# Performance work log

Measured on AMD Instinct MI355X. Metric: run time of the kernel, lower is better.

## Reference

```python
import jax, jax.numpy as jnp
import numpy as np

N, E, G = 100000, 400000, 4096
D, H, C, L = 128, 8, 16, 4  # hidden, heads, per-head dim, layers
EPS_BN = 1e-5


def _seg_sum(v, idx, n):
    return jax.ops.segment_sum(v, idx, num_segments=n)


def _seg_max(v, idx, n):
    return jax.ops.segment_max(v, idx, num_segments=n)


def setup_inputs() -> dict:
    key = jax.random.key(0)
    ks = jax.random.split(key, 32)
    rn = lambda k, s, sc=0.1: jax.random.normal(k, s, jnp.float32) * sc
    inp = {
        "x": jax.random.normal(ks[0], (N, 9), jnp.float32),
        "edge_attr": jax.random.normal(ks[1], (E, 3), jnp.float32),
        "edge_index": jax.random.randint(ks[2], (2, E), 0, N, jnp.int32),
        "batch": jnp.sort(jax.random.randint(ks[3], (N,), 0, G, jnp.int32)),
        "W_node": rn(ks[4], (9, D)), "b_node": jnp.zeros((D,), jnp.float32),
        "W_edge": rn(ks[5], (3, D)), "b_edge": jnp.zeros((D,), jnp.float32),
        "W_lin": rn(ks[6], (L, D, D)),
        "att_src": rn(ks[7], (L, H, C)), "att_dst": rn(ks[8], (L, H, C)),
        "W_eproj": rn(ks[9], (L, D, D)), "att_edge": rn(ks[10], (L, H, C)),
        "gat_bias": jnp.zeros((L, D), jnp.float32),
        "bn_gamma": jnp.ones((L, D), jnp.float32), "bn_beta": jnp.zeros((L, D), jnp.float32),
        "gate_W1": rn(ks[11], (D, D // 2)), "gate_b1": jnp.zeros((D // 2,), jnp.float32),
        "gate_W2": rn(ks[12], (D // 2, 1)), "gate_b2": jnp.zeros((1,), jnp.float32),
        "mlp_W1": rn(ks[13], (3 * D, 2 * D)), "mlp_b1": jnp.zeros((2 * D,), jnp.float32),
        "mlp_W2": rn(ks[14], (2 * D, D)), "mlp_b2": jnp.zeros((D,), jnp.float32),
    }
    return inp


def _forward(x, edge_attr, edge_index, batch, W_node, b_node, W_edge, b_edge,
             W_lin, att_src, att_dst, W_eproj, att_edge, gat_bias,
             bn_gamma, bn_beta, gate_W1, gate_b1, gate_W2, gate_b2,
             mlp_W1, mlp_b1, mlp_W2, mlp_b2):
    src, dst = edge_index[0], edge_index[1]
    h = x @ W_node + b_node                         # [N, D]
    e = edge_attr @ W_edge + b_edge                 # [E, D]

    # PyG add_self_loops(fill_value='mean'): self-loop edge feature = mean of
    # incoming edge features at each node.
    deg = _seg_sum(jnp.ones((E,), e.dtype), dst, N)           # [N]
    self_e = _seg_sum(e, dst, N) / jnp.clip(deg, 1.0)[:, None]  # [N, D]
    ar = jnp.arange(N, dtype=src.dtype)
    src_f = jnp.concatenate([src, ar])              # [E+N]
    dst_f = jnp.concatenate([dst, ar])
    e_f = jnp.concatenate([e, self_e], axis=0)      # [E+N, D]

    residual = h
    for l in range(L):
        hp = (h @ W_lin[l]).reshape(N, H, C)                     # [N, H, C]
        a_s = jnp.sum(hp * att_src[l], axis=-1)                  # [N, H]
        a_d = jnp.sum(hp * att_dst[l], axis=-1)                  # [N, H]
        ep = (e_f @ W_eproj[l]).reshape(-1, H, C)                # [E+N, H, C]
        a_e = jnp.sum(ep * att_edge[l], axis=-1)                 # [E+N, H]
        alpha = a_s[src_f] + a_d[dst_f] + a_e
        alpha = jax.nn.leaky_relu(alpha, negative_slope=0.2)
        # segment softmax over edges incident to each destination node
        m = _seg_max(alpha, dst_f, N)
        alpha = jnp.exp(alpha - m[dst_f])
        s = _seg_sum(alpha, dst_f, N)
        alpha = alpha / (s[dst_f] + 1e-16)                       # [E+N, H]
        msg = hp[src_f] * alpha[:, :, None]                      # [E+N, H, C]
        out = _seg_sum(msg, dst_f, N).reshape(N, D) + gat_bias[l]
        # BatchNorm1d (batch statistics, training-style) + ReLU
        mu = jnp.mean(out, axis=0)
        var = jnp.mean((out - mu) ** 2, axis=0)
        out = (out - mu) * jax.lax.rsqrt(var + EPS_BN) * bn_gamma[l] + bn_beta[l]
        out = jax.nn.relu(out)
        if l > 0 and l % 2 == 0:
            out = out + residual
            residual = out
        h = out

    # pooling
    cnt = _seg_sum(jnp.ones((N,), h.dtype), batch, G)            # [G]
    x_mean = _seg_sum(h, batch, G) / jnp.clip(cnt, 1.0)[:, None]
    x_max = _seg_max(h, batch, G)
    x_max = jnp.where(cnt[:, None] > 0, x_max, 0.0)
    gate = jax.nn.relu(h @ gate_W1 + gate_b1) @ gate_W2 + gate_b2  # [N, 1]
    gm = _seg_max(gate[:, 0], batch, G)
    gm = jnp.where(cnt > 0, gm, 0.0)
    ge = jnp.exp(gate[:, 0] - gm[batch])
    gs = _seg_sum(ge, batch, G)
    w = ge / (gs[batch] + 1e-16)
    x_att = _seg_sum(h * w[:, None], batch, G)                   # [G, D]

    gr = jnp.concatenate([x_mean, x_max, x_att], axis=1)         # [G, 3D]
    gr = jax.nn.relu(gr @ mlp_W1 + mlp_b1)
    return jax.nn.relu(gr @ mlp_W2 + mlp_b2)                     # [G, D]


def reference(x, edge_attr, edge_index, batch, W_node, b_node, W_edge, b_edge,
              W_lin, att_src, att_dst, W_eproj, att_edge, gat_bias,
              bn_gamma, bn_beta, gate_W1, gate_b1, gate_W2, gate_b2,
              mlp_W1, mlp_b1, mlp_W2, mlp_b2):
    return _forward(x, edge_attr, edge_index, batch, W_node, b_node, W_edge,
                    b_edge, W_lin, att_src, att_dst, W_eproj, att_edge,
                    gat_bias, bn_gamma, bn_beta, gate_W1, gate_b1, gate_W2,
                    gate_b2, mlp_W1, mlp_b1, mlp_W2, mlp_b2)
```

## Files before the change

### kernel.cpp

```cpp
#include <hip/hip_runtime.h>
#include <math.h>

#define N_NODES 100000
#define N_EDGES 400000
#define N_GRAPH 4096
#define DIM 128
#define HEADS 8
#define CHD 16
#define LAYERS 4
#define EPS_BN 1e-5f
#define BN_BLK 256

__global__ void k_prep(const float* __restrict__ W_eproj, const float* __restrict__ att_edge,
                       const float* __restrict__ W_edge, const float* __restrict__ b_edge,
                       float* __restrict__ small3, float* __restrict__ biasE) {
  __shared__ float sw[DIM * 32];
  int t = threadIdx.x;
  for (int e = t; e < DIM * 32; e += 256) {
    int d = e >> 5, lh = e & 31, l = lh >> 3, hh = lh & 7;
    float s = 0.f;
    const float* wp = W_eproj + ((size_t)l * DIM + d) * DIM + hh * CHD;
    const float* ap = att_edge + (l * HEADS + hh) * CHD;
    #pragma unroll
    for (int c = 0; c < CHD; ++c) s += wp[c] * ap[c];
    sw[e] = s;
  }
  __syncthreads();
  if (t < 96) {
    int l = t / 24, r = t % 24, k = r / 8, hh = r % 8;
    float s = 0.f;
    for (int d = 0; d < DIM; ++d) s += W_edge[k * DIM + d] * sw[d * 32 + l * 8 + hh];
    small3[t] = s;
  } else if (t < 128) {
    int t2 = t - 96, l = t2 / 8, hh = t2 % 8;
    float s = 0.f;
    for (int d = 0; d < DIM; ++d) s += b_edge[d] * sw[d * 32 + l * 8 + hh];
    biasE[t2] = s;
  }
}

__global__ void k_encode(const float* __restrict__ x, const float* __restrict__ Wn,
                         const float* __restrict__ bn, float* __restrict__ h,
                         float* __restrict__ resid) {
  __shared__ float sw[9 * DIM];
  __shared__ float sb[DIM];
  int t = threadIdx.x;
  for (int i = t; i < 9 * DIM; i += 256) sw[i] = Wn[i];
  if (t < DIM) sb[t] = bn[t];
  __syncthreads();
  size_t id = (size_t)blockIdx.x * 256 + t;
  if (id >= (size_t)N_NODES * DIM) return;
  int n = (int)(id >> 7), d = (int)(id & 127);
  float s = sb[d];
  const float* xr = x + (size_t)n * 9;
  #pragma unroll
  for (int k = 0; k < 9; ++k) s += xr[k] * sw[k * DIM + d];
  h[id] = s;
  resid[id] = s;
}

__global__ void k_deg(const int* __restrict__ dst, const float* __restrict__ ea,
                      int* __restrict__ deg, float* __restrict__ easum) {
  int i = blockIdx.x * 256 + threadIdx.x;
  if (i >= N_EDGES) return;
  int d = dst[i];
  atomicAdd(&deg[d], 1);
  atomicAdd(&easum[d * 3 + 0], ea[(size_t)i * 3 + 0]);
  atomicAdd(&easum[d * 3 + 1], ea[(size_t)i * 3 + 1]);
  atomicAdd(&easum[d * 3 + 2], ea[(size_t)i * 3 + 2]);
}

__global__ void k_scan1(const int* __restrict__ deg, int* __restrict__ rp, int* __restrict__ bsum) {
  __shared__ int s[256];
  int t = threadIdx.x, i = blockIdx.x * 256 + t;
  int v = (i < N_NODES) ? deg[i] : 0;
  s[t] = v;
  __syncthreads();
  for (int off = 1; off < 256; off <<= 1) {
    int u = (t >= off) ? s[t - off] : 0;
    __syncthreads();
    s[t] += u;
    __syncthreads();
  }
  if (i < N_NODES) rp[i] = s[t] - v;
  if (t == 255) bsum[blockIdx.x] = s[255];
}

__global__ void k_scan2(int* __restrict__ bsum, int nb) {
  __shared__ int s[512];
  int t = threadIdx.x;
  int v = (t < nb) ? bsum[t] : 0;
  s[t] = v;
  __syncthreads();
  for (int off = 1; off < 512; off <<= 1) {
    int u = (t >= off) ? s[t - off] : 0;
    __syncthreads();
    s[t] += u;
    __syncthreads();
  }
  if (t < nb) bsum[t] = s[t] - v;
}

__global__ void k_scan3(int* __restrict__ rp, const int* __restrict__ bsum) {
  int i = blockIdx.x * 256 + threadIdx.x;
  if (i < N_NODES) rp[i] += bsum[blockIdx.x];
  if (blockIdx.x == 0 && threadIdx.x == 0) rp[N_NODES] = N_EDGES;
}

__global__ void k_scatter(const int* __restrict__ src, const int* __restrict__ dst,
                          const int* __restrict__ rp, int* __restrict__ fill,
                          int* __restrict__ csrc, int* __restrict__ pos) {
  int i = blockIdx.x * 256 + threadIdx.x;
  if (i >= N_EDGES) return;
  int d = dst[i];
  int p = rp[d] + atomicAdd(&fill[d], 1);
  csrc[p] = src[i];
  pos[i] = p;
}

__launch_bounds__(256)
__global__ void k_gemm_hp(const float* __restrict__ h, const float* __restrict__ W,
                          const float* __restrict__ attS, const float* __restrict__ attD,
                          float* __restrict__ hp, float* __restrict__ a_s,
                          float* __restrict__ a_d) {
  __shared__ float sW[32 * DIM];
  __shared__ float sH[64 * 32];
  int t = threadIdx.x;
  int row0 = blockIdx.x * 64;
  int c0 = (t & 31) * 4;
  int r0 = (t >> 5) * 8;
  float acc[8][4] = {};
  for (int kk = 0; kk < DIM; kk += 32) {
    for (int e = t; e < 1024; e += 256) {
      int row = e >> 5, col4 = (e & 31) << 2;
      *reinterpret_cast<float4*>(&sW[row * DIM + col4]) =
          *reinterpret_cast<const float4*>(W + (size_t)(kk + row) * DIM + col4);
    }
    for (int e = t; e < 512; e += 256) {
      int rr = e >> 3, cc = (e & 7) << 2;
      int grr = row0 + rr;
      float4 v = (grr < N_NODES)
          ? *reinterpret_cast<const float4*>(h + (size_t)grr * DIM + kk + cc)
          : make_float4(0.f, 0.f, 0.f, 0.f);
      *reinterpret_cast<float4*>(&sH[rr * 32 + cc]) = v;
    }
    __syncthreads();
    #pragma unroll 4
    for (int k = 0; k < 32; ++k) {
      float4 wv = *reinterpret_cast<const float4*>(&sW[k * DIM + c0]);
      #pragma unroll
      for (int r = 0; r < 8; ++r) {
        float a = sH[(r0 + r) * 32 + k];
        acc[r][0] += a * wv.x; acc[r][1] += a * wv.y;
        acc[r][2] += a * wv.z; acc[r][3] += a * wv.w;
      }
    }
    __syncthreads();
  }
  int head = c0 >> 4;
  int cin = c0 & 15;
  const float* ap = attS + head * CHD + cin;
  const float* dp = attD + head * CHD + cin;
  float asw0 = ap[0], asw1 = ap[1], asw2 = ap[2], asw3 = ap[3];
  float adw0 = dp[0], adw1 = dp[1], adw2 = dp[2], adw3 = dp[3];
  #pragma unroll
  for (int r = 0; r < 8; ++r) {
    float ps = acc[r][0] * asw0 + acc[r][1] * asw1 + acc[r][2] * asw2 + acc[r][3] * asw3;
    float pd = acc[r][0] * adw0 + acc[r][1] * adw1 + acc[r][2] * adw2 + acc[r][3] * adw3;
    ps += __shfl_xor(ps, 1); ps += __shfl_xor(ps, 2);
    pd += __shfl_xor(pd, 1); pd += __shfl_xor(pd, 2);
    int n = row0 + r0 + r;
    if (n < N_NODES) {
      *reinterpret_cast<float4*>(hp + (size_t)n * DIM + c0) =
          make_float4(acc[r][0], acc[r][1], acc[r][2], acc[r][3]);
      if ((t & 3) == 0) {
        a_s[(size_t)n * HEADS + head] = ps;
        a_d[(size_t)n * HEADS + head] = pd;
      }
    }
  }
}

__global__ void k_alpha(const int* __restrict__ src, const int* __restrict__ dst,
                        const float* __restrict__ ea, const float* __restrict__ a_s,
                        const float* __restrict__ a_d, const float* __restrict__ easum,
                        const int* __restrict__ deg, const int* __restrict__ pos,
                        const float* __restrict__ small3, const float* __restrict__ biasE,
                        float* __restrict__ alpha, int l) {
  __shared__ float s3[24];
  __shared__ float sb[8];
  int t = threadIdx.x;
  if (t < 24) s3[t] = small3[l * 24 + t];
  else if (t < 32) sb[t - 24] = biasE[l * 8 + (t - 24)];
  __syncthreads();
  size_t i = (size_t)blockIdx.x * 256 + t;
  if (i >= (size_t)(N_EDGES + N_NODES)) return;
  float4 aslo, ashi, adlo, adhi;
  float ae[8];
  size_t wrow;
  if (i < N_EDGES) {
    int s = src[i], d = dst[i];
    wrow = (size_t)pos[i];
    float e0 = ea[i * 3 + 0], e1 = ea[i * 3 + 1], e2 = ea[i * 3 + 2];
    #pragma unroll
    for (int hh = 0; hh < 8; ++hh)
      ae[hh] = e0 * s3[hh] + e1 * s3[8 + hh] + e2 * s3[16 + hh] + sb[hh];
    aslo = *reinterpret_cast<const float4*>(a_s + (size_t)s * 8);
    ashi = *reinterpret_cast<const float4*>(a_s + (size_t)s * 8 + 4);
    adlo = *reinterpret_cast<const float4*>(a_d + (size_t)d * 8);
    adhi = *reinterpret_cast<const float4*>(a_d + (size_t)d * 8 + 4);
  } else {
    int n = (int)(i - N_EDGES);
    wrow = i;
    float e0 = easum[n * 3 + 0], e1 = easum[n * 3 + 1], e2 = easum[n * 3 + 2];
    float dg = (float)deg[n];
    float invd = 1.f / fmaxf(dg, 1.f);
    #pragma unroll
    for (int hh = 0; hh < 8; ++hh)
      ae[hh] = (e0 * s3[hh] + e1 * s3[8 + hh] + e2 * s3[16 + hh] + dg * sb[hh]) * invd;
    aslo = *reinterpret_cast<const float4*>(a_s + (size_t)n * 8);
    ashi = *reinterpret_cast<const float4*>(a_s + (size_t)n * 8 + 4);
    adlo = *reinterpret_cast<const float4*>(a_d + (size_t)n * 8);
    adhi = *reinterpret_cast<const float4*>(a_d + (size_t)n * 8 + 4);
  }
  float as8[8] = {aslo.x, aslo.y, aslo.z, aslo.w, ashi.x, ashi.y, ashi.z, ashi.w};
  float ad8[8] = {adlo.x, adlo.y, adlo.z, adlo.w, adhi.x, adhi.y, adhi.z, adhi.w};
  float o[8];
  #pragma unroll
  for (int hh = 0; hh < 8; ++hh) {
    float v = as8[hh] + ad8[hh] + ae[hh];
    o[hh] = (v > 0.f) ? v : 0.2f * v;
  }
  *reinterpret_cast<float4*>(alpha + wrow * 8) = make_float4(o[0], o[1], o[2], o[3]);
  *reinterpret_cast<float4*>(alpha + wrow * 8 + 4) = make_float4(o[4], o[5], o[6], o[7]);
}

__launch_bounds__(256)
__global__ void k_aggregate(const float* __restrict__ hp, const float* __restrict__ alpha,
                            const int* __restrict__ rp, const int* __restrict__ csrc,
                            const float* __restrict__ gbias, float* __restrict__ out) {
  int wv = threadIdx.x >> 6, lane = threadIdx.x & 63;
  int n = blockIdx.x * 4 + wv;
  if (n >= N_NODES) return;
  int p0 = rp[n], p1 = rp[n + 1];
  int deg = p1 - p0;
  int hh = lane & 7, sub = lane >> 3;
  const float* aself = alpha + (size_t)(N_EDGES + n) * 8;
  float m = aself[hh];
  for (int idx = sub; idx < deg; idx += 8)
    m = fmaxf(m, alpha[(size_t)(p0 + idx) * 8 + hh]);
  m = fmaxf(m, __shfl_xor(m, 8));
  m = fmaxf(m, __shfl_xor(m, 16));
  m = fmaxf(m, __shfl_xor(m, 32));
  float s = (sub == 0) ? expf(aself[hh] - m) : 0.f;
  for (int idx = sub; idx < deg; idx += 8)
    s += expf(alpha[(size_t)(p0 + idx) * 8 + hh] - m);
  s += __shfl_xor(s, 8); s += __shfl_xor(s, 16); s += __shfl_xor(s, 32);
  float inv = 1.f / (s + 1e-16f);
  int h0 = lane >> 4, h1 = h0 + 4;
  float m0 = __shfl(m, h0), m1 = __shfl(m, h1);
  float i0 = __shfl(inv, h0), i1 = __shfl(inv, h1);
  float w0 = expf(aself[h0] - m0) * i0;
  float w1 = expf(aself[h1] - m1) * i1;
  float acc0 = w0 * hp[(size_t)n * DIM + lane];
  float acc1 = w1 * hp[(size_t)n * DIM + 64 + lane];
  int idx = 0;
  for (; idx + 2 <= deg; idx += 2) {
    int sa = csrc[p0 + idx], sb2 = csrc[p0 + idx + 1];
    const float* ra = alpha + (size_t)(p0 + idx) * 8;
    const float* rb = alpha + (size_t)(p0 + idx + 1) * 8;
    float wa0 = expf(ra[h0] - m0) * i0, wa1 = expf(ra[h1] - m1) * i1;
    float wb0 = expf(rb[h0] - m0) * i0, wb1 = expf(rb[h1] - m1) * i1;
    acc0 += wa0 * hp[(size_t)sa * DIM + lane] + wb0 * hp[(size_t)sb2 * DIM + lane];
    acc1 += wa1 * hp[(size_t)sa * DIM + 64 + lane] + wb1 * hp[(size_t)sb2 * DIM + 64 + lane];
  }
  if (idx < deg) {
    int sa = csrc[p0 + idx];
    const float* ra = alpha + (size_t)(p0 + idx) * 8;
    float wa0 = expf(ra[h0] - m0) * i0, wa1 = expf(ra[h1] - m1) * i1;
    acc0 += wa0 * hp[(size_t)sa * DIM + lane];
    acc1 += wa1 * hp[(size_t)sa * DIM + 64 + lane];
  }
  out[(size_t)n * DIM + lane] = acc0 + gbias[lane];
  out[(size_t)n * DIM + 64 + lane] = acc1 + gbias[64 + lane];
}

__launch_bounds__(256)
__global__ void k_bnstat(const float* __restrict__ h, double* __restrict__ partial) {
  int t = threadIdx.x;
  int c = t & 127, half = t >> 7;
  double s = 0.0, q = 0.0;
  for (int n = blockIdx.x * 2 + half; n < N_NODES; n += BN_BLK * 2) {
    float v = h[(size_t)n * DIM + c];
    s += (double)v;
    q += (double)v * (double)v;
  }
  __shared__ double sd[512];
  sd[t] = s; sd[256 + t] = q;
  __syncthreads();
  if (t < 128) {
    s = sd[t] + sd[t + 128];
    q = sd[256 + t] + sd[256 + t + 128];
    partial[(size_t)blockIdx.x * 256 + t] = s;
    partial[(size_t)blockIdx.x * 256 + 128 + t] = q;
  }
}

__global__ void k_bnfin(const double* __restrict__ partial, const float* __restrict__ gamma,
                        const float* __restrict__ beta, float* __restrict__ ss) {
  int c = threadIdx.x;
  double s = 0.0, q = 0.0;
  for (int b = 0; b < BN_BLK; ++b) {
    s += partial[(size_t)b * 256 + c];
    q += partial[(size_t)b * 256 + 128 + c];
  }
  double mu = s / (double)N_NODES;
  double var = q / (double)N_NODES - mu * mu;
  if (var < 0.0) var = 0.0;
  float rs = rsqrtf((float)var + EPS_BN);
  float g = gamma[c] * rs;
  ss[c] = g;
  ss[DIM + c] = beta[c] - (float)mu * g;
}

__global__ void k_bnapply(float* __restrict__ h, const float* __restrict__ ss,
                          const float* __restrict__ resid, int addres) {
  size_t i = (size_t)blockIdx.x * 256 + threadIdx.x;
  if (i >= (size_t)N_NODES * DIM) return;
  int c = (int)(i & 127);
  float v = h[i] * ss[c] + ss[DIM + c];
  v = fmaxf(v, 0.f);
  if (addres) v += resid[i];
  h[i] = v;
}

__launch_bounds__(256, 2)
__global__ void k_gate(const float* __restrict__ h, const float* __restrict__ W1,
                       const float* __restrict__ b1, const float* __restrict__ W2,
                       const float* __restrict__ b2, float* __restrict__ gate) {
  __shared__ float sHT[128][64];
  __shared__ float red[16][64];
  int t = threadIdx.x;
  int row0 = blockIdx.x * 64;
  {
    int node = t & 63, kq = t >> 6;
    int gn = row0 + node;
    const float* hr = h + (size_t)gn * DIM + kq * 32;
    #pragma unroll
    for (int c = 0; c < 8; ++c) {
      float4 v = (gn < N_NODES) ? *reinterpret_cast<const float4*>(hr + c * 4)
                                : make_float4(0.f, 0.f, 0.f, 0.f);
      sHT[kq * 32 + c * 4 + 0][node] = v.x;
      sHT[kq * 32 + c * 4 + 1][node] = v.y;
      sHT[kq * 32 + c * 4 + 2][node] = v.z;
      sHT[kq * 32 + c * 4 + 3][node] = v.w;
    }
  }
  __syncthreads();
  int tx = t & 15, ty = t >> 4;
  float acc[4][4] = {};
  for (int k = 0; k < 128; k += 4) {
    float4 a0 = *reinterpret_cast<const float4*>(&sHT[k + 0][tx * 4]);
    float4 a1 = *reinterpret_cast<const float4*>(&sHT[k + 1][tx * 4]);
    float4 a2 = *reinterpret_cast<const float4*>(&sHT[k + 2][tx * 4]);
    float4 a3 = *reinterpret_cast<const float4*>(&sHT[k + 3][tx * 4]);
    float4 b0 = *reinterpret_cast<const float4*>(W1 + (size_t)(k + 0) * 64 + ty * 4);
    float4 b1v = *reinterpret_cast<const float4*>(W1 + (size_t)(k + 1) * 64 + ty * 4);
    float4 b2v = *reinterpret_cast<const float4*>(W1 + (size_t)(k + 2) * 64 + ty * 4);
    float4 b3v = *reinterpret_cast<const float4*>(W1 + (size_t)(k + 3) * 64 + ty * 4);
    const float ar[4][4] = {{a0.x, a0.y, a0.z, a0.w}, {a1.x, a1.y, a1.z, a1.w},
                            {a2.x, a2.y, a2.z, a2.w}, {a3.x, a3.y, a3.z, a3.w}};
    const float br[4][4] = {{b0.x, b0.y, b0.z, b0.w}, {b1v.x, b1v.y, b1v.z, b1v.w},
                            {b2v.x, b2v.y, b2v.z, b2v.w}, {b3v.x, b3v.y, b3v.z, b3v.w}};
    #pragma unroll
    for (int i = 0; i < 4; ++i)
      #pragma unroll
      for (int r = 0; r < 4; ++r)
        #pragma unroll
        for (int c = 0; c < 4; ++c)
          acc[r][c] += ar[i][r] * br[i][c];
  }
  float4 bb = *reinterpret_cast<const float4*>(b1 + ty * 4);
  float4 ww = *reinterpret_cast<const float4*>(W2 + ty * 4);
  #pragma unroll
  for (int r = 0; r < 4; ++r) {
    float p = fmaxf(acc[r][0] + bb.x, 0.f) * ww.x
            + fmaxf(acc[r][1] + bb.y, 0.f) * ww.y
            + fmaxf(acc[r][2] + bb.z, 0.f) * ww.z
            + fmaxf(acc[r][3] + bb.w, 0.f) * ww.w;
    red[ty][tx * 4 + r] = p;
  }
  __syncthreads();
  if (t < 64) {
    float ssum = b2[0];
    #pragma unroll
    for (int g = 0; g < 16; ++g) ssum += red[g][t];
    int n = row0 + t;
    if (n < N_NODES) gate[n] = ssum;
  }
}

__global__ void k_gptr(const int* __restrict__ batch, int* __restrict__ gptr) {
  int g = blockIdx.x * 256 + threadIdx.x;
  if (g > N_GRAPH) return;
  if (g == N_GRAPH) { gptr[g] = N_NODES; return; }
  int lo = 0, hi = N_NODES;
  while (lo < hi) {
    int mid = (lo + hi) >> 1;
    if (batch[mid] < g) lo = mid + 1; else hi = mid;
  }
  gptr[g] = lo;
}

__launch_bounds__(128)
__global__ void k_pool(const float* __restrict__ h, const float* __restrict__ gate,
                       const int* __restrict__ gptr, float* __restrict__ gr) {
  int g = blockIdx.x;
  int t = threadIdx.x;
  int p0 = gptr[g], p1 = gptr[g + 1], cnt = p1 - p0;
  float* out = gr + (size_t)g * 384;
  if (cnt == 0) { out[t] = 0.f; out[128 + t] = 0.f; out[256 + t] = 0.f; return; }
  __shared__ float red[2];
  __shared__ float wbuf[128];
  __shared__ float sgm, sinv;
  float lm = -1e30f;
  for (int n = p0 + t; n < p1; n += 128) lm = fmaxf(lm, gate[n]);
  for (int off = 1; off < 64; off <<= 1) lm = fmaxf(lm, __shfl_xor(lm, off));
  if ((t & 63) == 0) red[t >> 6] = lm;
  __syncthreads();
  if (t == 0) sgm = fmaxf(red[0], red[1]);
  __syncthreads();
  float gm = sgm;
  float ls = 0.f;
  for (int n = p0 + t; n < p1; n += 128) ls += expf(gate[n] - gm);
  for (int off = 1; off < 64; off <<= 1) ls += __shfl_xor(ls, off);
  if ((t & 63) == 0) red[t >> 6] = ls;
  __syncthreads();
  if (t == 0) sinv = 1.f / ((red[0] + red[1]) + 1e-16f);
  __syncthreads();
  float inv = sinv;
  float sm = 0.f, mx = -1e30f, wa = 0.f;
  for (int c0 = p0; c0 < p1; c0 += 128) {
    int lim = min(128, p1 - c0);
    if (t < lim) wbuf[t] = expf(gate[c0 + t] - gm) * inv;
    __syncthreads();
    for (int j = 0; j < lim; ++j) {
      float v = h[(size_t)(c0 + j) * DIM + t];
      sm += v;
      mx = fmaxf(mx, v);
      wa += v * wbuf[j];
    }
    __syncthreads();
  }
  out[t] = sm / (float)cnt;
  out[128 + t] = mx;
  out[256 + t] = wa;
}

__launch_bounds__(256)
__global__ void k_mlp1(const float* __restrict__ gr, const float* __restrict__ W1,
                       const float* __restrict__ b1, float* __restrict__ hid) {
  int j = threadIdx.x;
  int g0 = blockIdx.x * 8;
  float acc[8];
  float bj = b1[j];
  #pragma unroll
  for (int g = 0; g < 8; ++g) acc[g] = bj;
  for (int k = 0; k < 384; ++k) {
    float w = W1[(size_t)k * 256 + j];
    #pragma unroll
    for (int g = 0; g < 8; ++g) acc[g] += gr[(size_t)(g0 + g) * 384 + k] * w;
  }
  #pragma unroll
  for (int g = 0; g < 8; ++g) hid[(size_t)(g0 + g) * 256 + j] = fmaxf(acc[g], 0.f);
}

__launch_bounds__(128)
__global__ void k_mlp2(const float* __restrict__ hid, const float* __restrict__ W2,
                       const float* __restrict__ b2, float* __restrict__ out) {
  int j = threadIdx.x;
  int g0 = blockIdx.x * 8;
  float acc[8];
  float bj = b2[j];
  #pragma unroll
  for (int g = 0; g < 8; ++g) acc[g] = bj;
  for (int k = 0; k < 256; ++k) {
    float w = W2[(size_t)k * DIM + j];
    #pragma unroll
    for (int g = 0; g < 8; ++g) acc[g] += hid[(size_t)(g0 + g) * 256 + k] * w;
  }
  #pragma unroll
  for (int g = 0; g < 8; ++g) out[(size_t)(g0 + g) * DIM + j] = fmaxf(acc[g], 0.f);
}

extern "C" void kernel_launch(void* const* d_in, const int* in_sizes, int n_in,
                              void* d_out, int out_size, void* d_ws, size_t ws_size,
                              hipStream_t stream) {
  const float* x         = (const float*)d_in[0];
  const float* edge_attr = (const float*)d_in[1];
  const int*   eidx      = (const int*)d_in[2];
  const int*   batch     = (const int*)d_in[3];
  const float* W_node    = (const float*)d_in[4];
  const float* b_node    = (const float*)d_in[5];
  const float* W_edge    = (const float*)d_in[6];
  const float* b_edge    = (const float*)d_in[7];
  const float* W_lin     = (const float*)d_in[8];
  const float* att_src   = (const float*)d_in[9];
  const float* att_dst   = (const float*)d_in[10];
  const float* W_eproj   = (const float*)d_in[11];
  const float* att_edge  = (const float*)d_in[12];
  const float* gat_bias  = (const float*)d_in[13];
  const float* bn_gamma  = (const float*)d_in[14];
  const float* bn_beta   = (const float*)d_in[15];
  const float* gate_W1   = (const float*)d_in[16];
  const float* gate_b1   = (const float*)d_in[17];
  const float* gate_W2   = (const float*)d_in[18];
  const float* gate_b2   = (const float*)d_in[19];
  const float* mlp_W1    = (const float*)d_in[20];
  const float* mlp_b1    = (const float*)d_in[21];
  const float* mlp_W2    = (const float*)d_in[22];
  const float* mlp_b2    = (const float*)d_in[23];
  const int* src = eidx;
  const int* dst = eidx + N_EDGES;

  char* p = (char*)d_ws;
  auto take = [&](size_t bytes) -> char* {
    char* r = p;
    p += (bytes + 255) & ~(size_t)255;
    return r;
  };
  float* h      = (float*)take((size_t)N_NODES * DIM * 4);
  float* hp     = (float*)take((size_t)N_NODES * DIM * 4);
  float* resid  = (float*)take((size_t)N_NODES * DIM * 4);
  float* alpha  = (float*)take((size_t)(N_EDGES + N_NODES) * 8 * 4);
  float* a_s    = (float*)take((size_t)N_NODES * 8 * 4);
  float* a_d    = (float*)take((size_t)N_NODES * 8 * 4);
  char* zbase = p;
  float* easum  = (float*)take((size_t)N_NODES * 3 * 4);
  int*   deg    = (int*)take((size_t)N_NODES * 4);
  int*   fill   = (int*)take((size_t)N_NODES * 4);
  size_t zbytes = (size_t)(p - zbase);
  int*   rp     = (int*)take((size_t)(N_NODES + 1) * 4);
  int*   csrc   = (int*)take((size_t)N_EDGES * 4);
  int*   pos    = (int*)take((size_t)N_EDGES * 4);
  int*   bsum   = (int*)take(1024 * 4);
  float* small3 = (float*)take(96 * 4);
  float* biasE  = (float*)take(32 * 4);
  double* partial = (double*)take((size_t)BN_BLK * 256 * 8);
  float* ss     = (float*)take(256 * 4);
  float* gate   = (float*)take((size_t)N_NODES * 4);
  int*   gptr   = (int*)take((size_t)(N_GRAPH + 1) * 4);
  float* gr     = (float*)take((size_t)N_GRAPH * 384 * 4);
  float* hid    = (float*)take((size_t)N_GRAPH * 256 * 4);

  hipMemsetAsync(zbase, 0, zbytes, stream);
  k_prep<<<1, 256, 0, stream>>>(W_eproj, att_edge, W_edge, b_edge, small3, biasE);
  k_encode<<<(N_NODES * DIM) / 256, 256, 0, stream>>>(x, W_node, b_node, h, resid);
  k_deg<<<(N_EDGES + 255) / 256, 256, 0, stream>>>(dst, edge_attr, deg, easum);
  int nb = (N_NODES + 255) / 256;
  k_scan1<<<nb, 256, 0, stream>>>(deg, rp, bsum);
  k_scan2<<<1, 512, 0, stream>>>(bsum, nb);
  k_scan3<<<nb, 256, 0, stream>>>(rp, bsum);
  k_scatter<<<(N_EDGES + 255) / 256, 256, 0, stream>>>(src, dst, rp, fill, csrc, pos);

  for (int l = 0; l < LAYERS; ++l) {
    k_gemm_hp<<<(N_NODES + 63) / 64, 256, 0, stream>>>(
        h, W_lin + (size_t)l * DIM * DIM,
        att_src + l * HEADS * CHD, att_dst + l * HEADS * CHD, hp, a_s, a_d);
    k_alpha<<<(N_EDGES + N_NODES + 255) / 256, 256, 0, stream>>>(
        src, dst, edge_attr, a_s, a_d, easum, deg, pos, small3, biasE, alpha, l);
    k_aggregate<<<(N_NODES + 3) / 4, 256, 0, stream>>>(
        hp, alpha, rp, csrc, gat_bias + l * DIM, h);
    k_bnstat<<<BN_BLK, 256, 0, stream>>>(h, partial);
    k_bnfin<<<1, 128, 0, stream>>>(partial, bn_gamma + l * DIM, bn_beta + l * DIM, ss);
    k_bnapply<<<(N_NODES * DIM) / 256, 256, 0, stream>>>(h, ss, resid, (l == 2) ? 1 : 0);
  }

  k_gate<<<(N_NODES + 63) / 64, 256, 0, stream>>>(h, gate_W1, gate_b1, gate_W2, gate_b2, gate);
  k_gptr<<<(N_GRAPH + 1 + 255) / 256, 256, 0, stream>>>(batch, gptr);
  k_pool<<<N_GRAPH, 128, 0, stream>>>(h, gate, gptr, gr);
  k_mlp1<<<N_GRAPH / 8, 256, 0, stream>>>(gr, mlp_W1, mlp_b1, hid);
  k_mlp2<<<N_GRAPH / 8, 128, 0, stream>>>(hid, mlp_W2, mlp_b2, (float*)d_out);
}
```

Measured before the change: 1.309 ms.

## Fuse BN-apply into next GEMM load, CSR-sort edge data, single-pass aggregate

Removes the per-layer BN-apply pass by folding scale/shift, ReLU and the residual into the next layer's GEMM tile load, and applies BN only once at the end. Edge attributes and (src,dst) pairs are reordered into CSR order during scatter, so alpha is written contiguously and easum is computed by segmented reduction instead of atomics. Aggregation now does the softmax numerator and the weighted sum in one pass, broadcasting source indices with shuffles and normalising at the end. The GEMM inner loop is also vectorised with float4 reads of the H tile. The cost is extra work in the GEMM load and a serial per-node easum loop.

```diff
diff --git a/kernel.cpp b/kernel.cpp
--- a/kernel.cpp
+++ b/kernel.cpp
@@ -40,8 +40,7 @@
 }
 
 __global__ void k_encode(const float* __restrict__ x, const float* __restrict__ Wn,
-                         const float* __restrict__ bn, float* __restrict__ h,
-                         float* __restrict__ resid) {
+                         const float* __restrict__ bn, float* __restrict__ hEnc) {
   __shared__ float sw[9 * DIM];
   __shared__ float sb[DIM];
   int t = threadIdx.x;
@@ -55,19 +54,13 @@
   const float* xr = x + (size_t)n * 9;
   #pragma unroll
   for (int k = 0; k < 9; ++k) s += xr[k] * sw[k * DIM + d];
-  h[id] = s;
-  resid[id] = s;
-}
-
-__global__ void k_deg(const int* __restrict__ dst, const float* __restrict__ ea,
-                      int* __restrict__ deg, float* __restrict__ easum) {
+  hEnc[id] = s;
+}
+
+__global__ void k_deg(const int* __restrict__ dst, int* __restrict__ deg) {
   int i = blockIdx.x * 256 + threadIdx.x;
   if (i >= N_EDGES) return;
-  int d = dst[i];
-  atomicAdd(&deg[d], 1);
-  atomicAdd(&easum[d * 3 + 0], ea[(size_t)i * 3 + 0]);
-  atomicAdd(&easum[d * 3 + 1], ea[(size_t)i * 3 + 1]);
-  atomicAdd(&easum[d * 3 + 2], ea[(size_t)i * 3 + 2]);
+  atomicAdd(&deg[dst[i]], 1);
 }
 
 __global__ void k_scan1(const int* __restrict__ deg, int* __restrict__ rp, int* __restrict__ bsum) {
@@ -108,18 +101,39 @@
 }
 
 __global__ void k_scatter(const int* __restrict__ src, const int* __restrict__ dst,
-                          const int* __restrict__ rp, int* __restrict__ fill,
-                          int* __restrict__ csrc, int* __restrict__ pos) {
+                          const float* __restrict__ ea, const int* __restrict__ rp,
+                          int* __restrict__ fill, int2* __restrict__ cpair,
+                          float* __restrict__ cea) {
   int i = blockIdx.x * 256 + threadIdx.x;
   if (i >= N_EDGES) return;
   int d = dst[i];
   int p = rp[d] + atomicAdd(&fill[d], 1);
-  csrc[p] = src[i];
-  pos[i] = p;
+  cpair[p] = make_int2(src[i], d);
+  cea[(size_t)p * 3 + 0] = ea[(size_t)i * 3 + 0];
+  cea[(size_t)p * 3 + 1] = ea[(size_t)i * 3 + 1];
+  cea[(size_t)p * 3 + 2] = ea[(size_t)i * 3 + 2];
+}
+
+__global__ void k_easum(const int* __restrict__ rp, const float* __restrict__ cea,
+                        float* __restrict__ easum) {
+  int n = blockIdx.x * 256 + threadIdx.x;
+  if (n >= N_NODES) return;
+  int p0 = rp[n], p1 = rp[n + 1];
+  float s0 = 0.f, s1 = 0.f, s2 = 0.f;
+  for (int p = p0; p < p1; ++p) {
+    s0 += cea[(size_t)p * 3 + 0];
+    s1 += cea[(size_t)p * 3 + 1];
+    s2 += cea[(size_t)p * 3 + 2];
+  }
+  easum[n * 3 + 0] = s0;
+  easum[n * 3 + 1] = s1;
+  easum[n * 3 + 2] = s2;
 }
 
 __launch_bounds__(256)
-__global__ void k_gemm_hp(const float* __restrict__ h, const float* __restrict__ W,
+__global__ void k_gemm_hp(const float* __restrict__ hsrc, const float* __restrict__ hEnc,
+                          const float* __restrict__ ssv, int mode,
+                          const float* __restrict__ W,
                           const float* __restrict__ attS, const float* __restrict__ attD,
                           float* __restrict__ hp, float* __restrict__ a_s,
                           float* __restrict__ a_d) {
@@ -139,20 +153,39 @@
     for (int e = t; e < 512; e += 256) {
       int rr = e >> 3, cc = (e & 7) << 2;
       int grr = row0 + rr;
-      float4 v = (grr < N_NODES)
-          ? *reinterpret_cast<const float4*>(h + (size_t)grr * DIM + kk + cc)
-          : make_float4(0.f, 0.f, 0.f, 0.f);
+      int col = kk + cc;
+      float4 v = make_float4(0.f, 0.f, 0.f, 0.f);
+      if (grr < N_NODES) {
+        v = *reinterpret_cast<const float4*>(hsrc + (size_t)grr * DIM + col);
+        if (mode >= 1) {
+          float4 g = *reinterpret_cast<const float4*>(ssv + col);
+          float4 b = *reinterpret_cast<const float4*>(ssv + DIM + col);
+          v.x = fmaxf(v.x * g.x + b.x, 0.f);
+          v.y = fmaxf(v.y * g.y + b.y, 0.f);
+          v.z = fmaxf(v.z * g.z + b.z, 0.f);
+          v.w = fmaxf(v.w * g.w + b.w, 0.f);
+          if (mode == 2) {
+            float4 r4 = *reinterpret_cast<const float4*>(hEnc + (size_t)grr * DIM + col);
+            v.x += r4.x; v.y += r4.y; v.z += r4.z; v.w += r4.w;
+          }
+        }
+      }
       *reinterpret_cast<float4*>(&sH[rr * 32 + cc]) = v;
     }
     __syncthreads();
-    #pragma unroll 4
-    for (int k = 0; k < 32; ++k) {
-      float4 wv = *reinterpret_cast<const float4*>(&sW[k * DIM + c0]);
+    #pragma unroll 2
+    for (int k = 0; k < 32; k += 4) {
+      float4 w0 = *reinterpret_cast<const float4*>(&sW[(k + 0) * DIM + c0]);
+      float4 w1 = *reinterpret_cast<const float4*>(&sW[(k + 1) * DIM + c0]);
+      float4 w2 = *reinterpret_cast<const float4*>(&sW[(k + 2) * DIM + c0]);
+      float4 w3 = *reinterpret_cast<const float4*>(&sW[(k + 3) * DIM + c0]);
       #pragma unroll
       for (int r = 0; r < 8; ++r) {
-        float a = sH[(r0 + r) * 32 + k];
-        acc[r][0] += a * wv.x; acc[r][1] += a * wv.y;
-        acc[r][2] += a * wv.z; acc[r][3] += a * wv.w;
+        float4 a = *reinterpret_cast<const float4*>(&sH[(r0 + r) * 32 + k]);
+        acc[r][0] += a.x * w0.x; acc[r][0] += a.y * w1.x; acc[r][0] += a.z * w2.x; acc[r][0] += a.w * w3.x;
+        acc[r][1] += a.x * w0.y; acc[r][1] += a.y * w1.y; acc[r][1] += a.z * w2.y; acc[r][1] += a.w * w3.y;
+        acc[r][2] += a.x * w0.z; acc[r][2] += a.y * w1.z; acc[r][2] += a.z * w2.z; acc[r][2] += a.w * w3.z;
+        acc[r][3] += a.x * w0.w; acc[r][3] += a.y * w1.w; acc[r][3] += a.z * w2.w; acc[r][3] += a.w * w3.w;
       }
     }
     __syncthreads();
@@ -181,10 +214,9 @@
   }
 }
 
-__global__ void k_alpha(const int* __restrict__ src, const int* __restrict__ dst,
-                        const float* __restrict__ ea, const float* __restrict__ a_s,
-                        const float* __restrict__ a_d, const float* __restrict__ easum,
-                        const int* __restrict__ deg, const int* __restrict__ pos,
+__global__ void k_alpha(const int2* __restrict__ cpair, const float* __restrict__ cea,
+                        const float* __restrict__ a_s, const float* __restrict__ a_d,
+                        const float* __restrict__ easum, const int* __restrict__ rp,
                         const float* __restrict__ small3, const float* __restrict__ biasE,
                         float* __restrict__ alpha, int l) {
   __shared__ float s3[24];
@@ -197,23 +229,20 @@
   if (i >= (size_t)(N_EDGES + N_NODES)) return;
   float4 aslo, ashi, adlo, adhi;
   float ae[8];
-  size_t wrow;
   if (i < N_EDGES) {
-    int s = src[i], d = dst[i];
-    wrow = (size_t)pos[i];
-    float e0 = ea[i * 3 + 0], e1 = ea[i * 3 + 1], e2 = ea[i * 3 + 2];
+    int2 pr = cpair[i];
+    float e0 = cea[i * 3 + 0], e1 = cea[i * 3 + 1], e2 = cea[i * 3 + 2];
     #pragma unroll
     for (int hh = 0; hh < 8; ++hh)
       ae[hh] = e0 * s3[hh] + e1 * s3[8 + hh] + e2 * s3[16 + hh] + sb[hh];
-    aslo = *reinterpret_cast<const float4*>(a_s + (size_t)s * 8);
-    ashi = *reinterpret_cast<const float4*>(a_s + (size_t)s * 8 + 4);
-    adlo = *reinterpret_cast<const float4*>(a_d + (size_t)d * 8);
-    adhi = *reinterpret_cast<const float4*>(a_d + (size_t)d * 8 + 4);
+    aslo = *reinterpret_cast<const float4*>(a_s + (size_t)pr.x * 8);
+    ashi = *reinterpret_cast<const float4*>(a_s + (size_t)pr.x * 8 + 4);
+    adlo = *reinterpret_cast<const float4*>(a_d + (size_t)pr.y * 8);
+    adhi = *reinterpret_cast<const float4*>(a_d + (size_t)pr.y * 8 + 4);
   } else {
     int n = (int)(i - N_EDGES);
-    wrow = i;
     float e0 = easum[n * 3 + 0], e1 = easum[n * 3 + 1], e2 = easum[n * 3 + 2];
-    float dg = (float)deg[n];
+    float dg = (float)(rp[n + 1] - rp[n]);
     float invd = 1.f / fmaxf(dg, 1.f);
     #pragma unroll
     for (int hh = 0; hh < 8; ++hh)
@@ -231,13 +260,13 @@
     float v = as8[hh] + ad8[hh] + ae[hh];
     o[hh] = (v > 0.f) ? v : 0.2f * v;
   }
-  *reinterpret_cast<float4*>(alpha + wrow * 8) = make_float4(o[0], o[1], o[2], o[3]);
-  *reinterpret_cast<float4*>(alpha + wrow * 8 + 4) = make_float4(o[4], o[5], o[6], o[7]);
+  *reinterpret_cast<float4*>(alpha + i * 8) = make_float4(o[0], o[1], o[2], o[3]);
+  *reinterpret_cast<float4*>(alpha + i * 8 + 4) = make_float4(o[4], o[5], o[6], o[7]);
 }
 
 __launch_bounds__(256)
 __global__ void k_aggregate(const float* __restrict__ hp, const float* __restrict__ alpha,
-                            const int* __restrict__ rp, const int* __restrict__ csrc,
+                            const int* __restrict__ rp, const int2* __restrict__ cpair,
                             const float* __restrict__ gbias, float* __restrict__ out) {
   int wv = threadIdx.x >> 6, lane = threadIdx.x & 63;
   int n = blockIdx.x * 4 + wv;
@@ -252,37 +281,35 @@
   m = fmaxf(m, __shfl_xor(m, 8));
   m = fmaxf(m, __shfl_xor(m, 16));
   m = fmaxf(m, __shfl_xor(m, 32));
+  int h0 = lane >> 4, h1 = h0 + 4;
+  float m0 = __shfl(m, h0), m1 = __shfl(m, h1);
   float s = (sub == 0) ? expf(aself[hh] - m) : 0.f;
-  for (int idx = sub; idx < deg; idx += 8)
-    s += expf(alpha[(size_t)(p0 + idx) * 8 + hh] - m);
+  float acc0 = 0.f, acc1 = 0.f;
+  for (int j0 = 0; j0 < deg; j0 += 8) {
+    int idx = j0 + sub;
+    float e = 0.f;
+    int myc = 0;
+    if (idx < deg) {
+      e = expf(alpha[(size_t)(p0 + idx) * 8 + hh] - m);
+      myc = cpair[p0 + idx].x;
+    }
+    s += e;
+    int kmax = min(8, deg - j0);
+    for (int k = 0; k < kmax; ++k) {
+      int sa = __shfl(myc, k * 8);
+      float e0 = __shfl(e, k * 8 + h0);
+      float e1 = __shfl(e, k * 8 + h1);
+      acc0 += e0 * hp[(size_t)sa * DIM + lane];
+      acc1 += e1 * hp[(size_t)sa * DIM + 64 + lane];
+    }
+  }
   s += __shfl_xor(s, 8); s += __shfl_xor(s, 16); s += __shfl_xor(s, 32);
   float inv = 1.f / (s + 1e-16f);
-  int h0 = lane >> 4, h1 = h0 + 4;
-  float m0 = __shfl(m, h0), m1 = __shfl(m, h1);
   float i0 = __shfl(inv, h0), i1 = __shfl(inv, h1);
-  float w0 = expf(aself[h0] - m0) * i0;
-  float w1 = expf(aself[h1] - m1) * i1;
-  float acc0 = w0 * hp[(size_t)n * DIM + lane];
-  float acc1 = w1 * hp[(size_t)n * DIM + 64 + lane];
-  int idx = 0;
-  for (; idx + 2 <= deg; idx += 2) {
-    int sa = csrc[p0 + idx], sb2 = csrc[p0 + idx + 1];
-    const float* ra = alpha + (size_t)(p0 + idx) * 8;
-    const float* rb = alpha + (size_t)(p0 + idx + 1) * 8;
-    float wa0 = expf(ra[h0] - m0) * i0, wa1 = expf(ra[h1] - m1) * i1;
-    float wb0 = expf(rb[h0] - m0) * i0, wb1 = expf(rb[h1] - m1) * i1;
-    acc0 += wa0 * hp[(size_t)sa * DIM + lane] + wb0 * hp[(size_t)sb2 * DIM + lane];
-    acc1 += wa1 * hp[(size_t)sa * DIM + 64 + lane] + wb1 * hp[(size_t)sb2 * DIM + 64 + lane];
-  }
-  if (idx < deg) {
-    int sa = csrc[p0 + idx];
-    const float* ra = alpha + (size_t)(p0 + idx) * 8;
-    float wa0 = expf(ra[h0] - m0) * i0, wa1 = expf(ra[h1] - m1) * i1;
-    acc0 += wa0 * hp[(size_t)sa * DIM + lane];
-    acc1 += wa1 * hp[(size_t)sa * DIM + 64 + lane];
-  }
-  out[(size_t)n * DIM + lane] = acc0 + gbias[lane];
-  out[(size_t)n * DIM + 64 + lane] = acc1 + gbias[64 + lane];
+  acc0 += expf(aself[h0] - m0) * hp[(size_t)n * DIM + lane];
+  acc1 += expf(aself[h1] - m1) * hp[(size_t)n * DIM + 64 + lane];
+  out[(size_t)n * DIM + lane] = acc0 * i0 + gbias[lane];
+  out[(size_t)n * DIM + 64 + lane] = acc1 * i1 + gbias[64 + lane];
 }
 
 __launch_bounds__(256)
@@ -323,15 +350,12 @@
   ss[DIM + c] = beta[c] - (float)mu * g;
 }
 
-__global__ void k_bnapply(float* __restrict__ h, const float* __restrict__ ss,
-                          const float* __restrict__ resid, int addres) {
+__global__ void k_bnfinal(const float* __restrict__ hAgg, const float* __restrict__ ss,
+                          float* __restrict__ hFin) {
   size_t i = (size_t)blockIdx.x * 256 + threadIdx.x;
   if (i >= (size_t)N_NODES * DIM) return;
   int c = (int)(i & 127);
-  float v = h[i] * ss[c] + ss[DIM + c];
-  v = fmaxf(v, 0.f);
-  if (addres) v += resid[i];
-  h[i] = v;
+  hFin[i] = fmaxf(hAgg[i] * ss[c] + ss[DIM + c], 0.f);
 }
 
 __launch_bounds__(256, 2)
@@ -529,25 +553,25 @@
     p += (bytes + 255) & ~(size_t)255;
     return r;
   };
-  float* h      = (float*)take((size_t)N_NODES * DIM * 4);
+  float* hEnc   = (float*)take((size_t)N_NODES * DIM * 4);
+  float* hAgg   = (float*)take((size_t)N_NODES * DIM * 4);
   float* hp     = (float*)take((size_t)N_NODES * DIM * 4);
-  float* resid  = (float*)take((size_t)N_NODES * DIM * 4);
   float* alpha  = (float*)take((size_t)(N_EDGES + N_NODES) * 8 * 4);
   float* a_s    = (float*)take((size_t)N_NODES * 8 * 4);
   float* a_d    = (float*)take((size_t)N_NODES * 8 * 4);
+  int2*  cpair  = (int2*)take((size_t)N_EDGES * 8);
+  float* cea    = (float*)take((size_t)N_EDGES * 3 * 4);
+  float* easum  = (float*)take((size_t)N_NODES * 3 * 4);
   char* zbase = p;
-  float* easum  = (float*)take((size_t)N_NODES * 3 * 4);
   int*   deg    = (int*)take((size_t)N_NODES * 4);
   int*   fill   = (int*)take((size_t)N_NODES * 4);
   size_t zbytes = (size_t)(p - zbase);
   int*   rp     = (int*)take((size_t)(N_NODES + 1) * 4);
-  int*   csrc   = (int*)take((size_t)N_EDGES * 4);
-  int*   pos    = (int*)take((size_t)N_EDGES * 4);
   int*   bsum   = (int*)take(1024 * 4);
   float* small3 = (float*)take(96 * 4);
   float* biasE  = (float*)take(32 * 4);
   double* partial = (double*)take((size_t)BN_BLK * 256 * 8);
-  float* ss     = (float*)take(256 * 4);
+  float* ssAll  = (float*)take(4 * 256 * 4);
   float* gate   = (float*)take((size_t)N_NODES * 4);
   int*   gptr   = (int*)take((size_t)(N_GRAPH + 1) * 4);
   float* gr     = (float*)take((size_t)N_GRAPH * 384 * 4);
@@ -555,30 +579,36 @@
 
   hipMemsetAsync(zbase, 0, zbytes, stream);
   k_prep<<<1, 256, 0, stream>>>(W_eproj, att_edge, W_edge, b_edge, small3, biasE);
-  k_encode<<<(N_NODES * DIM) / 256, 256, 0, stream>>>(x, W_node, b_node, h, resid);
-  k_deg<<<(N_EDGES + 255) / 256, 256, 0, stream>>>(dst, edge_attr, deg, easum);
+  k_encode<<<(N_NODES * DIM) / 256, 256, 0, stream>>>(x, W_node, b_node, hEnc);
+  k_deg<<<(N_EDGES + 255) / 256, 256, 0, stream>>>(dst, deg);
   int nb = (N_NODES + 255) / 256;
   k_scan1<<<nb, 256, 0, stream>>>(deg, rp, bsum);
   k_scan2<<<1, 512, 0, stream>>>(bsum, nb);
   k_scan3<<<nb, 256, 0, stream>>>(rp, bsum);
-  k_scatter<<<(N_EDGES + 255) / 256, 256, 0, stream>>>(src, dst, rp, fill, csrc, pos);
+  k_scatter<<<(N_EDGES + 255) / 256, 256, 0, stream>>>(src, dst, edge_attr, rp, fill, cpair, cea);
+  k_easum<<<nb, 256, 0, stream>>>(rp, cea, easum);
 
   for (int l = 0; l < LAYERS; ++l) {
+    const float* hsrc = (l == 0) ? hEnc : hAgg;
+    int mode = (l == 0) ? 0 : ((l == 3) ? 2 : 1);
     k_gemm_hp<<<(N_NODES + 63) / 64, 256, 0, stream>>>(
-        h, W_lin + (size_t)l * DIM * DIM,
+        hsrc, hEnc, ssAll + (l > 0 ? (l - 1) * 256 : 0), mode,
+        W_lin + (size_t)l * DIM * DIM,
         att_src + l * HEADS * CHD, att_dst + l * HEADS * CHD, hp, a_s, a_d);
     k_alpha<<<(N_EDGES + N_NODES + 255) / 256, 256, 0, stream>>>(
-        src, dst, edge_attr, a_s, a_d, easum, deg, pos, small3, biasE, alpha, l);
+        cpair, cea, a_s, a_d, easum, rp, small3, biasE, alpha, l);
     k_aggregate<<<(N_NODES + 3) / 4, 256, 0, stream>>>(
-        hp, alpha, rp, csrc, gat_bias + l * DIM, h);
-    k_bnstat<<<BN_BLK, 256, 0, stream>>>(h, partial);
-    k_bnfin<<<1, 128, 0, stream>>>(partial, bn_gamma + l * DIM, bn_beta + l * DIM, ss);
-    k_bnapply<<<(N_NODES * DIM) / 256, 256, 0, stream>>>(h, ss, resid, (l == 2) ? 1 : 0);
-  }
-
-  k_gate<<<(N_NODES + 63) / 64, 256, 0, stream>>>(h, gate_W1, gate_b1, gate_W2, gate_b2, gate);
+        hp, alpha, rp, cpair, gat_bias + l * DIM, hAgg);
+    k_bnstat<<<BN_BLK, 256, 0, stream>>>(hAgg, partial);
+    k_bnfin<<<1, 128, 0, stream>>>(partial, bn_gamma + l * DIM, bn_beta + l * DIM,
+                                   ssAll + l * 256);
+  }
+
+  float* hFin = hp;
+  k_bnfinal<<<(N_NODES * DIM) / 256, 256, 0, stream>>>(hAgg, ssAll + 3 * 256, hFin);
+  k_gate<<<(N_NODES + 63) / 64, 256, 0, stream>>>(hFin, gate_W1, gate_b1, gate_W2, gate_b2, gate);
   k_gptr<<<(N_GRAPH + 1 + 255) / 256, 256, 0, stream>>>(batch, gptr);
-  k_pool<<<N_GRAPH, 128, 0, stream>>>(h, gate, gptr, gr);
+  k_pool<<<N_GRAPH, 128, 0, stream>>>(hFin, gate, gptr, gr);
   k_mlp1<<<N_GRAPH / 8, 256, 0, stream>>>(gr, mlp_W1, mlp_b1, hid);
   k_mlp2<<<N_GRAPH / 8, 128, 0, stream>>>(hid, mlp_W2, mlp_b2, (float*)d_out);
 }
```

Result: faster. 1.139 ms (-13.0%).
